# Performance work log

Hardware: AMD Instinct MI355X
Metric: run time of the kernel (lower is better)

Reference implementation:

```python
import jax, jax.numpy as jnp
import numpy as np

B, S, D, H = 2, 2048, 1024, 16
HD = D // H

def setup_inputs() -> dict:
    key = jax.random.key(0)
    ks = jax.random.split(key, 6)
    X = jax.random.normal(ks[0], (B, S, D), dtype=jnp.float32)
    mask = jax.random.randint(ks[1], (B, 1, S, S), 0, 2, dtype=jnp.int32)
    scale = 1.0 / np.sqrt(D)
    Wq = jax.random.normal(ks[2], (D, D), dtype=jnp.float32) * scale
    Wk = jax.random.normal(ks[3], (D, D), dtype=jnp.float32) * scale
    Wv = jax.random.normal(ks[4], (D, D), dtype=jnp.float32) * scale
    Wo = jax.random.normal(ks[5], (D, D), dtype=jnp.float32) * scale
    return {"X": X, "mask": mask, "Wq": Wq, "Wk": Wk, "Wv": Wv, "Wo": Wo}

def reference(X, mask, Wq, Wk, Wv, Wo):
    b, s, d = X.shape
    # torch nn.Linear(bias=False): y = x @ W.T, W is [out, in]
    def split_heads(Y):
        return Y.reshape(b, s, H, HD).transpose(0, 2, 1, 3)  # [b,h,s,hd]
    Q = split_heads(X @ Wq.T)
    K = split_heads(X @ Wk.T)
    V = split_heads(X @ Wv.T)
    scores = jnp.einsum('bhqd,bhkd->bhqk', Q, K) / jnp.sqrt(jnp.float32(HD))
    # Faithful to original: masked positions filled with -1e-09 (sic)
    scores = jnp.where(mask == 0, jnp.float32(-1e-09), scores)
    # dropout p=0.0 -> identity (applied to scores pre-softmax in original)
    weights = jax.nn.softmax(scores, axis=-1)
    out = jnp.einsum('bhqk,bhkd->bhqd', weights, V)  # [b,h,s,hd]
    out = out.transpose(0, 2, 1, 3).reshape(b, s, d)
    return out @ Wo.T
```

## Files before the change

### kernel.cpp

```cpp
#include <hip/hip_runtime.h>
#include <hip/hip_bf16.h>

using short8  = __attribute__((ext_vector_type(8))) short;
using short4v = __attribute__((ext_vector_type(4))) short;
using f32x4   = __attribute__((ext_vector_type(4))) float;

__device__ __forceinline__ unsigned short f2bf(float x){
  union { float f; unsigned u; } c; c.f = x;
  unsigned u = c.u + 0x7FFFu + ((c.u >> 16) & 1u);
  return (unsigned short)(u >> 16);
}

__device__ __forceinline__ unsigned pack_bf16_rn(float a, float b){
  __hip_bfloat162 t = __float22bfloat162_rn(make_float2(a, b));
  unsigned u; __builtin_memcpy(&u, &t, 4);
  return u;
}

__global__ void cvt4(const float* __restrict__ src, unsigned short* __restrict__ dst,
                     int n, float scale){
  int i = (blockIdx.x * blockDim.x + threadIdx.x) * 4;
  if (i >= n) return;
  float4 v = *(const float4*)(src + i);
  ushort4 o;
  o.x = f2bf(v.x * scale); o.y = f2bf(v.y * scale);
  o.z = f2bf(v.z * scale); o.w = f2bf(v.w * scale);
  *(ushort4*)(dst + i) = o;
}

__global__ void cvt_mask(const int* __restrict__ src, unsigned char* __restrict__ dst, int n){
  int i = (blockIdx.x * blockDim.x + threadIdx.x) * 4;
  if (i >= n) return;
  int4 v = *(const int4*)(src + i);
  unsigned out = (v.x ? 1u : 0u) | ((v.y ? 1u : 0u) << 8) |
                 ((v.z ? 1u : 0u) << 16) | ((v.w ? 1u : 0u) << 24);
  *(unsigned*)(dst + i) = out;
}

__device__ __forceinline__ void stage16(const unsigned short* g, unsigned short* l){
  __builtin_amdgcn_global_load_lds(
      (const __attribute__((address_space(1))) void*)g,
      (__attribute__((address_space(3))) void*)l, 16, 0, 0);
}

template<bool F32OUT>
__global__ __launch_bounds__(256) void gemm_bt(const unsigned short* __restrict__ A,
                                               const unsigned short* __restrict__ B,
                                               unsigned short* __restrict__ Cb,
                                               float* __restrict__ Cf,
                                               int M, int N, int K)
{
  __shared__ unsigned short As[128*32];
  __shared__ unsigned short Bs[128*32];
  const int tid = threadIdx.x;
  const int wave = tid >> 6, lane = tid & 63, l16 = lane & 15, quad = lane >> 4;
  const int bm = blockIdx.x * 128, bn = blockIdx.y * 128;
  const int wm = (wave >> 1) * 64, wn = (wave & 1) * 64;

  f32x4 acc[4][4] = {};

  for (int k0 = 0; k0 < K; k0 += 32){
    #pragma unroll
    for (int c = 0; c < 2; c++){
      int idx = c * 256 + tid;
      int row = idx >> 2, g = (idx & 3) * 8;
      stage16(A + (size_t)(bm + row) * K + k0 + g, &As[idx * 8]);
      stage16(B + (size_t)(bn + row) * K + k0 + g, &Bs[idx * 8]);
    }
    __syncthreads();
    short8 af[4], bf[4];
    #pragma unroll
    for (int i = 0; i < 4; i++) af[i] = *(const short8*)&As[(wm + i*16 + l16)*32 + quad*8];
    #pragma unroll
    for (int j = 0; j < 4; j++) bf[j] = *(const short8*)&Bs[(wn + j*16 + l16)*32 + quad*8];
    #pragma unroll
    for (int i = 0; i < 4; i++)
      #pragma unroll
      for (int j = 0; j < 4; j++)
        acc[i][j] = __builtin_amdgcn_mfma_f32_16x16x32_bf16(af[i], bf[j], acc[i][j], 0, 0, 0);
    __syncthreads();
  }

  #pragma unroll
  for (int i = 0; i < 4; i++){
    int mrow = bm + wm + i*16 + quad*4;
    #pragma unroll
    for (int j = 0; j < 4; j++){
      int ncol = bn + wn + j*16 + l16;
      #pragma unroll
      for (int r = 0; r < 4; r++){
        if (F32OUT) Cf[(size_t)(mrow + r) * N + ncol] = acc[i][j][r];
        else        Cb[(size_t)(mrow + r) * N + ncol] = f2bf(acc[i][j][r]);
      }
    }
  }
}

__global__ __launch_bounds__(256) void vtrans(const unsigned short* __restrict__ QKV,
                                              unsigned short* __restrict__ Vg)
{
  __shared__ unsigned T[64 * 33];
  const int tid = threadIdx.x;
  const int sblk = blockIdx.x, bh = blockIdx.y, b = bh >> 4, h = bh & 15;
  const unsigned short* src = QKV + (size_t)(b*2048 + sblk*64) * 3072 + 2048 + h*64;

  {
    int sp = tid >> 3, dg = (tid & 7) * 8;
    short8 v0 = *(const short8*)(src + (size_t)(2*sp    ) * 3072 + dg);
    short8 v1 = *(const short8*)(src + (size_t)(2*sp + 1) * 3072 + dg);
    #pragma unroll
    for (int j = 0; j < 8; j++){
      unsigned pair = ((unsigned)(unsigned short)v0[j]) | (((unsigned)(unsigned short)v1[j]) << 16);
      T[(dg + j) * 33 + sp] = pair;
    }
  }
  __syncthreads();
  {
    int d = tid >> 2, spg = (tid & 3) * 8;
    unsigned tmp[8];
    #pragma unroll
    for (int j = 0; j < 8; j++) tmp[j] = T[d * 33 + spg + j];
    unsigned short* dst = Vg + ((size_t)bh*64 + d) * 2048 + sblk*64 + spg*2;
    *(short8*)(dst)     = *(short8*)&tmp[0];
    *(short8*)(dst + 8) = *(short8*)&tmp[4];
  }
}

__global__ __launch_bounds__(256) void attn(const unsigned short* __restrict__ QKV,
                                            const unsigned short* __restrict__ Vg,
                                            const unsigned char* __restrict__ mask8,
                                            unsigned short* __restrict__ O)
{
  __shared__ char smem[17408];
  unsigned short* Ks = (unsigned short*)smem;
  unsigned short* Vt = (unsigned short*)(smem + 8192);
  float* lsums = (float*)(smem + 16384);
  float* red   = (float*)smem;

  const int tid = threadIdx.x, wave = tid >> 6, lane = tid & 63;
  const int l16 = lane & 15, quad = lane >> 4;
  const int bh = blockIdx.y, b = bh >> 4, h = bh & 15;
  const int qblk = blockIdx.x * 64;
  const unsigned short* Qbase = QKV + (size_t)b * 2048 * 3072 + h * 64;
  const unsigned short* Kbase = Qbase + 1024;
  const unsigned short* Vbase = Vg + (size_t)bh * 64 * 2048;
  const unsigned char*  mbase = mask8 + (size_t)b * 2048 * 2048;

  short8 qf[4][2];
  #pragma unroll
  for (int nt = 0; nt < 4; nt++)
    #pragma unroll
    for (int ks = 0; ks < 2; ks++)
      qf[nt][ks] = *(const short8*)(Qbase + (size_t)(qblk + nt*16 + l16) * 3072 + ks*32 + quad*8);

  f32x4 oacc[4][4] = {};
  float plsum[4] = {0.f, 0.f, 0.f, 0.f};
  const int sw = l16 & 7;

  for (int j0 = 0; j0 < 2048; j0 += 64){
    __syncthreads();
    #pragma unroll
    for (int it = 0; it < 2; it++){
      int s = it * 256 + tid;
      int row = s >> 3, blk = s & 7, bg = blk ^ (row & 7);
      stage16(Kbase + (size_t)(j0 + row) * 3072 + bg * 8, Ks + s * 8);
      stage16(Vbase + (size_t)row * 2048 + j0 + bg * 8, Vt + s * 8);
    }
    __syncthreads();

    short8 kf0 = *(const short8*)&Ks[(wave*16 + l16) * 64 + ((0*4 + quad) ^ sw) * 8];
    short8 kf1 = *(const short8*)&Ks[(wave*16 + l16) * 64 + ((1*4 + quad) ^ sw) * 8];
    f32x4 sacc[4];
    #pragma unroll
    for (int nt = 0; nt < 4; nt++){
      f32x4 a = {0.f, 0.f, 0.f, 0.f};
      a = __builtin_amdgcn_mfma_f32_16x16x32_bf16(kf0, qf[nt][0], a, 0, 0, 0);
      a = __builtin_amdgcn_mfma_f32_16x16x32_bf16(kf1, qf[nt][1], a, 0, 0, 0);
      sacc[nt] = a;
    }

    short4v b2[4];
    const int kbyte = j0 + wave*16 + quad*4;
    #pragma unroll
    for (int nt = 0; nt < 4; nt++){
      unsigned md = *(const unsigned*)(mbase + (size_t)(qblk + nt*16 + l16) * 2048 + kbyte);
      float p0 = __expf(sacc[nt][0] * (float)( md        & 255u));
      float p1 = __expf(sacc[nt][1] * (float)((md >>  8) & 255u));
      float p2 = __expf(sacc[nt][2] * (float)((md >> 16) & 255u));
      float p3 = __expf(sacc[nt][3] * (float)( md >> 24        ));
      plsum[nt] += (p0 + p1) + (p2 + p3);
      unsigned u0 = pack_bf16_rn(p0, p1), u1 = pack_bf16_rn(p2, p3);
      union { unsigned u[2]; short4v s; } pk; pk.u[0] = u0; pk.u[1] = u1;
      b2[nt] = pk.s;
    }

    #pragma unroll
    for (int dt = 0; dt < 4; dt++){
      int physb = (wave*2 + (quad >> 1)) ^ sw;
      short4v a2 = *(const short4v*)&Vt[(dt*16 + l16) * 64 + physb * 8 + (quad & 1) * 4];
      #pragma unroll
      for (int nt = 0; nt < 4; nt++)
        oacc[dt][nt] = __builtin_amdgcn_mfma_f32_16x16x16bf16_1k(a2, b2[nt], oacc[dt][nt], 0, 0, 0);
    }
  }

  float lw[4];
  #pragma unroll
  for (int nt = 0; nt < 4; nt++){
    float v = plsum[nt];
    v += __shfl_xor(v, 16);
    v += __shfl_xor(v, 32);
    lw[nt] = v;
  }
  __syncthreads();
  if (quad == 0){
    #pragma unroll
    for (int nt = 0; nt < 4; nt++) lsums[wave*64 + nt*16 + l16] = lw[nt];
  }
  if (wave == 0){
    #pragma unroll
    for (int dt = 0; dt < 4; dt++)
      #pragma unroll
      for (int nt = 0; nt < 4; nt++)
        *(f32x4*)&red[((dt*4 + nt)*64 + lane)*4] = oacc[dt][nt];
  }
  __syncthreads();
  for (int w = 1; w <= 2; w++){
    if (wave == w){
      #pragma unroll
      for (int dt = 0; dt < 4; dt++)
        #pragma unroll
        for (int nt = 0; nt < 4; nt++){
          f32x4* p = (f32x4*)&red[((dt*4 + nt)*64 + lane)*4];
          *p = *p + oacc[dt][nt];
        }
    }
    __syncthreads();
  }
  if (wave == 3){
    float linv[4];
    #pragma unroll
    for (int nt = 0; nt < 4; nt++){
      int q = nt*16 + l16;
      linv[nt] = 1.0f / (lsums[q] + lsums[64 + q] + lsums[128 + q] + lsums[192 + q]);
    }
    #pragma unroll
    for (int dt = 0; dt < 4; dt++)
      #pragma unroll
      for (int nt = 0; nt < 4; nt++){
        f32x4 t = *(f32x4*)&red[((dt*4 + nt)*64 + lane)*4];
        t = t + oacc[dt][nt];
        unsigned u0 = pack_bf16_rn(t[0] * linv[nt], t[1] * linv[nt]);
        unsigned u1 = pack_bf16_rn(t[2] * linv[nt], t[3] * linv[nt]);
        uint2 st; st.x = u0; st.y = u1;
        *(uint2*)&O[(size_t)(b*2048 + qblk + nt*16 + l16) * 1024 + h*64 + dt*16 + quad*4] = st;
      }
  }
}

extern "C" void kernel_launch(void* const* d_in, const int* in_sizes, int n_in,
                              void* d_out, int out_size, void* d_ws, size_t ws_size,
                              hipStream_t stream)
{
  const float* X  = (const float*)d_in[0];
  const int*   Mk = (const int*)d_in[1];
  const float* Wq = (const float*)d_in[2];
  const float* Wk = (const float*)d_in[3];
  const float* Wv = (const float*)d_in[4];
  const float* Wo = (const float*)d_in[5];
  float* out = (float*)d_out;

  char* ws = (char*)d_ws;
  unsigned short* Xb   = (unsigned short*)(ws + 0);
  unsigned short* Wqkv = (unsigned short*)(ws + 8388608);
  unsigned short* Wob  = (unsigned short*)(ws + 14680064);
  unsigned short* QKV  = (unsigned short*)(ws + 16777216);
  unsigned short* Ob   = (unsigned short*)(ws + 41943040);
  unsigned char*  M8   = (unsigned char*) (ws + 50331648);
  unsigned short* Vg   = (unsigned short*)(ws + 58720256);

  cvt4<<<4096, 256, 0, stream>>>(X,  Xb,              4194304, 1.0f);
  cvt4<<<1024, 256, 0, stream>>>(Wq, Wqkv,            1048576, 0.125f);
  cvt4<<<1024, 256, 0, stream>>>(Wk, Wqkv + 1048576,  1048576, 1.0f);
  cvt4<<<1024, 256, 0, stream>>>(Wv, Wqkv + 2097152,  1048576, 1.0f);
  cvt4<<<1024, 256, 0, stream>>>(Wo, Wob,             1048576, 1.0f);
  cvt_mask<<<8192, 256, 0, stream>>>(Mk, M8, 8388608);

  gemm_bt<false><<<dim3(32, 24), 256, 0, stream>>>(Xb, Wqkv, QKV, nullptr, 4096, 3072, 1024);
  vtrans<<<dim3(32, 32), 256, 0, stream>>>(QKV, Vg);
  attn<<<dim3(32, 32), 256, 0, stream>>>(QKV, Vg, M8, Ob);
  gemm_bt<true><<<dim3(32, 8), 256, 0, stream>>>(Ob, Wob, nullptr, out, 4096, 1024, 1024);
}
```

Before: 295.0 us.

## Fuse prep kernels, write transposed V from QKV GEMM, widen attention key tile

Merges the six conversion launches into one prep kernel, and removes the separate V-transpose kernel by having the QKV GEMM epilogue write V directly in transposed layout. The attention kernel now stages Q into LDS instead of registers and processes 128 keys per iteration with two sub-tiles. It also uses exp2 with the log2e factor folded into the Wq scale. This cuts launch overhead, one pass over V, and half the barrier count per key, at the cost of more LDS and scattered 8-byte V stores.

New measurement: 429.9 us. 45.7% more time.

```diff
diff --git a/kernel.cpp b/kernel.cpp
--- a/kernel.cpp
+++ b/kernel.cpp
@@ -4,6 +4,12 @@
 using short8  = __attribute__((ext_vector_type(8))) short;
 using short4v = __attribute__((ext_vector_type(4))) short;
 using f32x4   = __attribute__((ext_vector_type(4))) float;
+
+#if __has_builtin(__builtin_amdgcn_exp2f)
+#define EXP2(x) __builtin_amdgcn_exp2f(x)
+#else
+#define EXP2(x) __expf(0.6931471805599453f*(x))
+#endif
 
 __device__ __forceinline__ unsigned short f2bf(float x){
   union { float f; unsigned u; } c; c.f = x;
@@ -17,24 +23,32 @@
   return u;
 }
 
-__global__ void cvt4(const float* __restrict__ src, unsigned short* __restrict__ dst,
-                     int n, float scale){
-  int i = (blockIdx.x * blockDim.x + threadIdx.x) * 4;
-  if (i >= n) return;
-  float4 v = *(const float4*)(src + i);
-  ushort4 o;
-  o.x = f2bf(v.x * scale); o.y = f2bf(v.y * scale);
-  o.z = f2bf(v.z * scale); o.w = f2bf(v.w * scale);
-  *(ushort4*)(dst + i) = o;
-}
-
-__global__ void cvt_mask(const int* __restrict__ src, unsigned char* __restrict__ dst, int n){
-  int i = (blockIdx.x * blockDim.x + threadIdx.x) * 4;
-  if (i >= n) return;
-  int4 v = *(const int4*)(src + i);
-  unsigned out = (v.x ? 1u : 0u) | ((v.y ? 1u : 0u) << 8) |
-                 ((v.z ? 1u : 0u) << 16) | ((v.w ? 1u : 0u) << 24);
-  *(unsigned*)(dst + i) = out;
+__global__ __launch_bounds__(256) void prep(const float* __restrict__ X, const int* __restrict__ Mk,
+                                            const float* __restrict__ Wq, const float* __restrict__ Wk,
+                                            const float* __restrict__ Wv, const float* __restrict__ Wo,
+                                            unsigned short* __restrict__ Xb, unsigned short* __restrict__ Wqkv,
+                                            unsigned short* __restrict__ Wob, unsigned char* __restrict__ M8)
+{
+  const int bid = blockIdx.x, tid = threadIdx.x;
+  if (bid < 8192){
+    const float* src; unsigned short* dst; float scale; int i;
+    if (bid < 4096)      { src = X;  dst = Xb;             scale = 1.0f;          i = bid*1024 + tid*4; }
+    else if (bid < 5120) { src = Wq; dst = Wqkv;           scale = 0.18033688f;   i = (bid-4096)*1024 + tid*4; }
+    else if (bid < 6144) { src = Wk; dst = Wqkv + 1048576; scale = 1.0f;          i = (bid-5120)*1024 + tid*4; }
+    else if (bid < 7168) { src = Wv; dst = Wqkv + 2097152; scale = 1.0f;          i = (bid-6144)*1024 + tid*4; }
+    else                 { src = Wo; dst = Wob;            scale = 1.0f;          i = (bid-7168)*1024 + tid*4; }
+    float4 v = *(const float4*)(src + i);
+    ushort4 o;
+    o.x = f2bf(v.x * scale); o.y = f2bf(v.y * scale);
+    o.z = f2bf(v.z * scale); o.w = f2bf(v.w * scale);
+    *(ushort4*)(dst + i) = o;
+  } else {
+    int i = (bid - 8192)*1024 + tid*4;
+    int4 v = *(const int4*)(Mk + i);
+    unsigned out = (v.x ? 1u : 0u) | ((v.y ? 1u : 0u) << 8) |
+                   ((v.z ? 1u : 0u) << 16) | ((v.w ? 1u : 0u) << 24);
+    *(unsigned*)(M8 + i) = out;
+  }
 }
 
 __device__ __forceinline__ void stage16(const unsigned short* g, unsigned short* l){
@@ -43,12 +57,10 @@
       (__attribute__((address_space(3))) void*)l, 16, 0, 0);
 }
 
-template<bool F32OUT>
-__global__ __launch_bounds__(256) void gemm_bt(const unsigned short* __restrict__ A,
-                                               const unsigned short* __restrict__ B,
-                                               unsigned short* __restrict__ Cb,
-                                               float* __restrict__ Cf,
-                                               int M, int N, int K)
+__global__ __launch_bounds__(256) void gemm_qkv(const unsigned short* __restrict__ A,
+                                                const unsigned short* __restrict__ B,
+                                                unsigned short* __restrict__ C,
+                                                unsigned short* __restrict__ Vg)
 {
   __shared__ unsigned short As[128*32];
   __shared__ unsigned short Bs[128*32];
@@ -56,9 +68,9 @@
   const int wave = tid >> 6, lane = tid & 63, l16 = lane & 15, quad = lane >> 4;
   const int bm = blockIdx.x * 128, bn = blockIdx.y * 128;
   const int wm = (wave >> 1) * 64, wn = (wave & 1) * 64;
+  const int K = 1024;
 
   f32x4 acc[4][4] = {};
-
   for (int k0 = 0; k0 < K; k0 += 32){
     #pragma unroll
     for (int c = 0; c < 2; c++){
@@ -81,6 +93,70 @@
     __syncthreads();
   }
 
+  if (bn < 2048){
+    #pragma unroll
+    for (int i = 0; i < 4; i++){
+      int mrow = bm + wm + i*16 + quad*4;
+      #pragma unroll
+      for (int j = 0; j < 4; j++){
+        int ncol = bn + wn + j*16 + l16;
+        #pragma unroll
+        for (int r = 0; r < 4; r++)
+          C[(size_t)(mrow + r) * 3072 + ncol] = f2bf(acc[i][j][r]);
+      }
+    }
+  } else {
+    #pragma unroll
+    for (int i = 0; i < 4; i++){
+      int srow = bm + wm + i*16 + quad*4;
+      int b = srow >> 11, s = srow & 2047;
+      #pragma unroll
+      for (int j = 0; j < 4; j++){
+        int c = bn - 2048 + wn + j*16 + l16;
+        int h = c >> 6, d = c & 63;
+        ushort4 o;
+        o.x = f2bf(acc[i][j][0]); o.y = f2bf(acc[i][j][1]);
+        o.z = f2bf(acc[i][j][2]); o.w = f2bf(acc[i][j][3]);
+        *(ushort4*)&Vg[((size_t)(b*16 + h)*64 + d) * 2048 + s] = o;
+      }
+    }
+  }
+}
+
+__global__ __launch_bounds__(256) void gemm_out(const unsigned short* __restrict__ A,
+                                                const unsigned short* __restrict__ B,
+                                                float* __restrict__ Cf)
+{
+  __shared__ unsigned short As[128*32];
+  __shared__ unsigned short Bs[128*32];
+  const int tid = threadIdx.x;
+  const int wave = tid >> 6, lane = tid & 63, l16 = lane & 15, quad = lane >> 4;
+  const int bm = blockIdx.x * 128, bn = blockIdx.y * 128;
+  const int wm = (wave >> 1) * 64, wn = (wave & 1) * 64;
+  const int K = 1024, N = 1024;
+
+  f32x4 acc[4][4] = {};
+  for (int k0 = 0; k0 < K; k0 += 32){
+    #pragma unroll
+    for (int c = 0; c < 2; c++){
+      int idx = c * 256 + tid;
+      int row = idx >> 2, g = (idx & 3) * 8;
+      stage16(A + (size_t)(bm + row) * K + k0 + g, &As[idx * 8]);
+      stage16(B + (size_t)(bn + row) * K + k0 + g, &Bs[idx * 8]);
+    }
+    __syncthreads();
+    short8 af[4], bf[4];
+    #pragma unroll
+    for (int i = 0; i < 4; i++) af[i] = *(const short8*)&As[(wm + i*16 + l16)*32 + quad*8];
+    #pragma unroll
+    for (int j = 0; j < 4; j++) bf[j] = *(const short8*)&Bs[(wn + j*16 + l16)*32 + quad*8];
+    #pragma unroll
+    for (int i = 0; i < 4; i++)
+      #pragma unroll
+      for (int j = 0; j < 4; j++)
+        acc[i][j] = __builtin_amdgcn_mfma_f32_16x16x32_bf16(af[i], bf[j], acc[i][j], 0, 0, 0);
+    __syncthreads();
+  }
   #pragma unroll
   for (int i = 0; i < 4; i++){
     int mrow = bm + wm + i*16 + quad*4;
@@ -88,119 +164,88 @@
     for (int j = 0; j < 4; j++){
       int ncol = bn + wn + j*16 + l16;
       #pragma unroll
-      for (int r = 0; r < 4; r++){
-        if (F32OUT) Cf[(size_t)(mrow + r) * N + ncol] = acc[i][j][r];
-        else        Cb[(size_t)(mrow + r) * N + ncol] = f2bf(acc[i][j][r]);
-      }
-    }
-  }
-}
-
-__global__ __launch_bounds__(256) void vtrans(const unsigned short* __restrict__ QKV,
-                                              unsigned short* __restrict__ Vg)
-{
-  __shared__ unsigned T[64 * 33];
-  const int tid = threadIdx.x;
-  const int sblk = blockIdx.x, bh = blockIdx.y, b = bh >> 4, h = bh & 15;
-  const unsigned short* src = QKV + (size_t)(b*2048 + sblk*64) * 3072 + 2048 + h*64;
-
-  {
-    int sp = tid >> 3, dg = (tid & 7) * 8;
-    short8 v0 = *(const short8*)(src + (size_t)(2*sp    ) * 3072 + dg);
-    short8 v1 = *(const short8*)(src + (size_t)(2*sp + 1) * 3072 + dg);
-    #pragma unroll
-    for (int j = 0; j < 8; j++){
-      unsigned pair = ((unsigned)(unsigned short)v0[j]) | (((unsigned)(unsigned short)v1[j]) << 16);
-      T[(dg + j) * 33 + sp] = pair;
-    }
-  }
-  __syncthreads();
-  {
-    int d = tid >> 2, spg = (tid & 3) * 8;
-    unsigned tmp[8];
-    #pragma unroll
-    for (int j = 0; j < 8; j++) tmp[j] = T[d * 33 + spg + j];
-    unsigned short* dst = Vg + ((size_t)bh*64 + d) * 2048 + sblk*64 + spg*2;
-    *(short8*)(dst)     = *(short8*)&tmp[0];
-    *(short8*)(dst + 8) = *(short8*)&tmp[4];
-  }
-}
-
-__global__ __launch_bounds__(256) void attn(const unsigned short* __restrict__ QKV,
-                                            const unsigned short* __restrict__ Vg,
-                                            const unsigned char* __restrict__ mask8,
-                                            unsigned short* __restrict__ O)
-{
-  __shared__ char smem[17408];
+      for (int r = 0; r < 4; r++)
+        Cf[(size_t)(mrow + r) * N + ncol] = acc[i][j][r];
+    }
+  }
+}
+
+__global__ __launch_bounds__(256, 4) void attn(const unsigned short* __restrict__ QKV,
+                                               const unsigned short* __restrict__ Vg,
+                                               const unsigned char* __restrict__ mask8,
+                                               unsigned short* __restrict__ O)
+{
+  __shared__ char smem[40960];
   unsigned short* Ks = (unsigned short*)smem;
-  unsigned short* Vt = (unsigned short*)(smem + 8192);
+  unsigned short* Vt = (unsigned short*)(smem + 16384);
+  unsigned short* Qs = (unsigned short*)(smem + 32768);
+  float* red   = (float*)smem;
   float* lsums = (float*)(smem + 16384);
-  float* red   = (float*)smem;
 
   const int tid = threadIdx.x, wave = tid >> 6, lane = tid & 63;
   const int l16 = lane & 15, quad = lane >> 4;
   const int bh = blockIdx.y, b = bh >> 4, h = bh & 15;
   const int qblk = blockIdx.x * 64;
-  const unsigned short* Qbase = QKV + (size_t)b * 2048 * 3072 + h * 64;
-  const unsigned short* Kbase = Qbase + 1024;
-  const unsigned short* Vbase = Vg + (size_t)bh * 64 * 2048;
+  const unsigned short* Qg  = QKV + (size_t)b * 2048 * 3072 + h * 64;
+  const unsigned short* Kg  = Qg + 1024;
+  const unsigned short* Vgb = Vg + (size_t)bh * 64 * 2048;
   const unsigned char*  mbase = mask8 + (size_t)b * 2048 * 2048;
 
-  short8 qf[4][2];
   #pragma unroll
-  for (int nt = 0; nt < 4; nt++)
-    #pragma unroll
-    for (int ks = 0; ks < 2; ks++)
-      qf[nt][ks] = *(const short8*)(Qbase + (size_t)(qblk + nt*16 + l16) * 3072 + ks*32 + quad*8);
+  for (int it = 0; it < 2; it++){
+    int s = it * 256 + tid;
+    int row = s >> 3, bg = (s & 7) ^ (row & 7);
+    stage16(Qg + (size_t)(qblk + row) * 3072 + bg * 8, Qs + s * 8);
+  }
 
   f32x4 oacc[4][4] = {};
   float plsum[4] = {0.f, 0.f, 0.f, 0.f};
-  const int sw = l16 & 7;
-
-  for (int j0 = 0; j0 < 2048; j0 += 64){
-    __syncthreads();
-    #pragma unroll
-    for (int it = 0; it < 2; it++){
+
+  for (int j0 = 0; j0 < 2048; j0 += 128){
+    __syncthreads();
+    #pragma unroll
+    for (int it = 0; it < 4; it++){
       int s = it * 256 + tid;
-      int row = s >> 3, blk = s & 7, bg = blk ^ (row & 7);
-      stage16(Kbase + (size_t)(j0 + row) * 3072 + bg * 8, Ks + s * 8);
-      stage16(Vbase + (size_t)row * 2048 + j0 + bg * 8, Vt + s * 8);
-    }
-    __syncthreads();
-
-    short8 kf0 = *(const short8*)&Ks[(wave*16 + l16) * 64 + ((0*4 + quad) ^ sw) * 8];
-    short8 kf1 = *(const short8*)&Ks[(wave*16 + l16) * 64 + ((1*4 + quad) ^ sw) * 8];
-    f32x4 sacc[4];
-    #pragma unroll
-    for (int nt = 0; nt < 4; nt++){
-      f32x4 a = {0.f, 0.f, 0.f, 0.f};
-      a = __builtin_amdgcn_mfma_f32_16x16x32_bf16(kf0, qf[nt][0], a, 0, 0, 0);
-      a = __builtin_amdgcn_mfma_f32_16x16x32_bf16(kf1, qf[nt][1], a, 0, 0, 0);
-      sacc[nt] = a;
-    }
-
-    short4v b2[4];
-    const int kbyte = j0 + wave*16 + quad*4;
-    #pragma unroll
-    for (int nt = 0; nt < 4; nt++){
-      unsigned md = *(const unsigned*)(mbase + (size_t)(qblk + nt*16 + l16) * 2048 + kbyte);
-      float p0 = __expf(sacc[nt][0] * (float)( md        & 255u));
-      float p1 = __expf(sacc[nt][1] * (float)((md >>  8) & 255u));
-      float p2 = __expf(sacc[nt][2] * (float)((md >> 16) & 255u));
-      float p3 = __expf(sacc[nt][3] * (float)( md >> 24        ));
-      plsum[nt] += (p0 + p1) + (p2 + p3);
-      unsigned u0 = pack_bf16_rn(p0, p1), u1 = pack_bf16_rn(p2, p3);
-      union { unsigned u[2]; short4v s; } pk; pk.u[0] = u0; pk.u[1] = u1;
-      b2[nt] = pk.s;
-    }
-
-    #pragma unroll
-    for (int dt = 0; dt < 4; dt++){
-      int physb = (wave*2 + (quad >> 1)) ^ sw;
-      short4v a2 = *(const short4v*)&Vt[(dt*16 + l16) * 64 + physb * 8 + (quad & 1) * 4];
-      #pragma unroll
-      for (int nt = 0; nt < 4; nt++)
-        oacc[dt][nt] = __builtin_amdgcn_mfma_f32_16x16x16bf16_1k(a2, b2[nt], oacc[dt][nt], 0, 0, 0);
+      int krow = s >> 3, kb = (s & 7) ^ (krow & 7);
+      stage16(Kg + (size_t)(j0 + krow) * 3072 + kb * 8, Ks + s * 8);
+      int vrow = s >> 4, vb = (s & 15) ^ (vrow & 7);
+      stage16(Vgb + (size_t)vrow * 2048 + j0 + vb * 8, Vt + s * 8);
+    }
+    __syncthreads();
+
+    #pragma unroll
+    for (int kt = 0; kt < 2; kt++){
+      const int krow = wave*32 + kt*16 + l16;
+      short8 kf0 = *(const short8*)&Ks[krow*64 + ((0 + quad) ^ (krow & 7))*8];
+      short8 kf1 = *(const short8*)&Ks[krow*64 + ((4 + quad) ^ (krow & 7))*8];
+      short4v b2[4];
+      #pragma unroll
+      for (int nt = 0; nt < 4; nt++){
+        const int qrow = nt*16 + l16;
+        short8 qf0 = *(const short8*)&Qs[qrow*64 + ((0 + quad) ^ (qrow & 7))*8];
+        short8 qf1 = *(const short8*)&Qs[qrow*64 + ((4 + quad) ^ (qrow & 7))*8];
+        f32x4 a = {0.f, 0.f, 0.f, 0.f};
+        a = __builtin_amdgcn_mfma_f32_16x16x32_bf16(kf0, qf0, a, 0, 0, 0);
+        a = __builtin_amdgcn_mfma_f32_16x16x32_bf16(kf1, qf1, a, 0, 0, 0);
+        unsigned md = *(const unsigned*)(mbase + (size_t)(qblk + qrow) * 2048 + j0 + wave*32 + kt*16 + quad*4);
+        float p0 = EXP2(a[0] * (float)( md        & 255u));
+        float p1 = EXP2(a[1] * (float)((md >>  8) & 255u));
+        float p2 = EXP2(a[2] * (float)((md >> 16) & 255u));
+        float p3 = EXP2(a[3] * (float)( md >> 24        ));
+        plsum[nt] += (p0 + p1) + (p2 + p3);
+        union { unsigned u[2]; short4v s4; } pk;
+        pk.u[0] = pack_bf16_rn(p0, p1); pk.u[1] = pack_bf16_rn(p2, p3);
+        b2[nt] = pk.s4;
+      }
+      #pragma unroll
+      for (int dt = 0; dt < 4; dt++){
+        const int drow = dt*16 + l16;
+        int pb = (wave*4 + kt*2 + (quad >> 1)) ^ (drow & 7);
+        short4v a2 = *(const short4v*)&Vt[drow*128 + pb*8 + (quad & 1)*4];
+        #pragma unroll
+        for (int nt = 0; nt < 4; nt++)
+          oacc[dt][nt] = __builtin_amdgcn_mfma_f32_16x16x16bf16_1k(a2, b2[nt], oacc[dt][nt], 0, 0, 0);
+      }
     }
   }
 
@@ -279,15 +324,8 @@
   unsigned char*  M8   = (unsigned char*) (ws + 50331648);
   unsigned short* Vg   = (unsigned short*)(ws + 58720256);
 
-  cvt4<<<4096, 256, 0, stream>>>(X,  Xb,              4194304, 1.0f);
-  cvt4<<<1024, 256, 0, stream>>>(Wq, Wqkv,            1048576, 0.125f);
-  cvt4<<<1024, 256, 0, stream>>>(Wk, Wqkv + 1048576,  1048576, 1.0f);
-  cvt4<<<1024, 256, 0, stream>>>(Wv, Wqkv + 2097152,  1048576, 1.0f);
-  cvt4<<<1024, 256, 0, stream>>>(Wo, Wob,             1048576, 1.0f);
-  cvt_mask<<<8192, 256, 0, stream>>>(Mk, M8, 8388608);
-
-  gemm_bt<false><<<dim3(32, 24), 256, 0, stream>>>(Xb, Wqkv, QKV, nullptr, 4096, 3072, 1024);
-  vtrans<<<dim3(32, 32), 256, 0, stream>>>(QKV, Vg);
+  prep<<<16384, 256, 0, stream>>>(X, Mk, Wq, Wk, Wv, Wo, Xb, Wqkv, Wob, M8);
+  gemm_qkv<<<dim3(32, 24), 256, 0, stream>>>(Xb, Wqkv, QKV, Vg);
   attn<<<dim3(32, 32), 256, 0, stream>>>(QKV, Vg, M8, Ob);
-  gemm_bt<true><<<dim3(32, 8), 256, 0, stream>>>(Ob, Wob, nullptr, out, 4096, 1024, 1024);
-}
+  gemm_out<<<dim3(32, 8), 256, 0, stream>>>(Ob, Wob, out);
+}
```
